# Performance work log

Measured on AMD Instinct MI355X. Metric: run time of the kernel, lower is better.

Reference implementation:

```python
import jax, jax.numpy as jnp
import numpy as np

NUM_HEADS = 16
EMBED_DIM = 1024
HEAD_DIM = EMBED_DIM // NUM_HEADS
REG_LEN = 2048
SUM_LEN = 64
BSZ = 2
REL_DIM = 64
NUM_REL_EMB = 64
MAX_SUMMARY = 64
SCALE = HEAD_DIM ** -0.5


def _ln(x, g, b, eps=1e-5):
    m = jnp.mean(x, axis=-1, keepdims=True)
    v = jnp.mean((x - m) ** 2, axis=-1, keepdims=True)
    return (x - m) * jax.lax.rsqrt(v + eps) * g + b


def setup_inputs() -> dict:
    key = jax.random.key(0)
    ks = jax.random.split(key, 16)
    inp = {}
    inp['reg_x'] = jax.random.normal(ks[0], (REG_LEN, BSZ, EMBED_DIM), jnp.float32)
    inp['sum_token_ids'] = jax.random.randint(ks[1], (BSZ, SUM_LEN), 0, MAX_SUMMARY + 1)
    inp['rel_idx'] = jax.random.randint(ks[2], (BSZ, SUM_LEN + REG_LEN, REG_LEN), 0, NUM_REL_EMB)
    inp['sum_len'] = SUM_LEN
    inp['reg_len'] = REG_LEN
    emb = jax.random.normal(ks[3], (MAX_SUMMARY + 1, EMBED_DIM), jnp.float32) * 0.02
    inp['emb_sum'] = emb.at[0].set(0.0)  # padding_idx = 0
    inp['rel_emb0'] = jax.random.normal(ks[4], (NUM_REL_EMB, REL_DIM), jnp.float32) * 0.02

    def lin(k, din, dout):
        return jax.random.normal(k, (din, dout), jnp.float32) * (1.0 / np.sqrt(din))

    inp['Wq'] = lin(ks[5], EMBED_DIM, EMBED_DIM); inp['bq'] = jnp.zeros((EMBED_DIM,), jnp.float32)
    inp['Wk'] = lin(ks[6], EMBED_DIM, EMBED_DIM); inp['bk'] = jnp.zeros((EMBED_DIM,), jnp.float32)
    inp['Wv'] = lin(ks[7], EMBED_DIM, EMBED_DIM); inp['bv'] = jnp.zeros((EMBED_DIM,), jnp.float32)
    inp['Wr0'] = lin(ks[8], REL_DIM, EMBED_DIM); inp['br0'] = jnp.zeros((EMBED_DIM,), jnp.float32)
    inp['Wk2'] = lin(ks[9], HEAD_DIM, HEAD_DIM); inp['bk2'] = jnp.zeros((HEAD_DIM,), jnp.float32)
    inp['Wv2'] = lin(ks[10], HEAD_DIM, HEAD_DIM); inp['bv2'] = jnp.zeros((HEAD_DIM,), jnp.float32)
    inp['Wo'] = lin(ks[11], EMBED_DIM, EMBED_DIM); inp['bo'] = jnp.zeros((EMBED_DIM,), jnp.float32)
    for name in ['ln_k', 'ln_v', 'ln_k2', 'ln_v2']:
        inp[name + '_g'] = jnp.ones((HEAD_DIM,), jnp.float32)
        inp[name + '_b'] = jnp.zeros((HEAD_DIM,), jnp.float32)
    return inp


def reference(reg_x, sum_token_ids, rel_idx, sum_len, reg_len, emb_sum, rel_emb0,
              Wq, bq, Wk, bk, Wv, bv, Wr0, br0, Wk2, bk2, Wv2, bv2, Wo, bo,
              ln_k_g, ln_k_b, ln_v_g, ln_v_b, ln_k2_g, ln_k2_b, ln_v2_g, ln_v2_b):
    R, B, E = reg_x.shape  # reg_len, bsz, embed_dim
    H, D = NUM_HEADS, HEAD_DIM
    S = sum_token_ids.shape[1]

    # regular K/V projections + per-head LayerNorm
    reg_k = _ln((reg_x @ Wk + bk).reshape(R, B, H, D), ln_k_g, ln_k_b)
    reg_v = _ln((reg_x @ Wv + bv).reshape(R, B, H, D), ln_v_g, ln_v_b)

    # relation-type embedding projection -> [Rrel, H, D]
    r0 = (rel_emb0 @ Wr0 + br0).reshape(NUM_REL_EMB, H, D)

    # --- stage 1: summary tokens attend over regular tokens ---
    sum_x = emb_sum[sum_token_ids.T]                     # [S, B, E]
    sum_q = sum_x.reshape(S, B, H, D) * SCALE
    scores_sum = jnp.einsum('sbhd,kbhd->bhsk', sum_q, reg_k)   # [B,H,S,R]
    qr_sum = jnp.einsum('sbhd,Zhd->bhsZ', sum_q, r0)           # [B,H,S,Rrel]
    idx_sum = rel_idx[:, :S]                                   # [B,S,R]
    scores_sum = scores_sum + jnp.take_along_axis(qr_sum, idx_sum[:, None, :, :], axis=-1)
    w_sum = jax.nn.softmax(scores_sum, axis=-1)
    sum_x2 = jnp.einsum('bhsk,kbhd->sbhd', w_sum, reg_v)       # [S,B,H,D]

    sum_k2 = _ln(sum_x2 @ Wk2 + bk2, ln_k2_g, ln_k2_b)
    sum_v2 = _ln(sum_x2 @ Wv2 + bv2, ln_v2_g, ln_v2_b)

    # --- stage 2: regular tokens attend over [summary ; regular] keys ---
    reg_q = (reg_x @ Wq + bq).reshape(R, B, H, D) * SCALE
    scores_rs = jnp.einsum('qbhd,sbhd->bhqs', reg_q, sum_k2)   # [B,H,R,S]
    scores_rr = jnp.einsum('qbhd,kbhd->bhqk', reg_q, reg_k)    # [B,H,R,R]
    qr_reg = jnp.einsum('qbhd,Zhd->bhqZ', reg_q, r0)
    idx_reg = rel_idx[:, S:]                                   # [B,R,R]
    scores_rr = scores_rr + jnp.take_along_axis(qr_reg, idx_reg[:, None, :, :], axis=-1)
    scores = jnp.concatenate([scores_rs, scores_rr], axis=-1)  # [B,H,R,S+R]
    w = jax.nn.softmax(scores, axis=-1)
    v_all = jnp.concatenate([sum_v2, reg_v], axis=0)           # [S+R,B,H,D]
    attn_out = jnp.einsum('bhqk,kbhd->qbhd', w, v_all).reshape(R, B, E)
    reg_x2 = attn_out @ Wo + bo
    return reg_x2
```

## Files before the change

kernel.cpp:

```cpp
#include <hip/hip_runtime.h>
#include <cstdint>
#include <cstddef>

#define NH   16
#define HD   64
#define RLEN 2048
#define BSZ  2
#define SLEN 64
#define NZ   64
#define ED   1024
#define KTOT 2112
#define NSPLIT 8

typedef __bf16 bf16_t;
typedef bf16_t bf16x8 __attribute__((ext_vector_type(8)));
typedef bf16_t bf16x4 __attribute__((ext_vector_type(4)));
typedef float  f32x4  __attribute__((ext_vector_type(4)));

__device__ __forceinline__ f32x4 mfma16(bf16x8 a, bf16x8 b, f32x4 c) {
    return __builtin_amdgcn_mfma_f32_16x16x32_bf16(a, b, c, 0, 0, 0);
}

__device__ __forceinline__ void dma16(const void* g, void* l) {
    __builtin_amdgcn_global_load_lds(
        (const __attribute__((address_space(1))) unsigned int*)g,
        (__attribute__((address_space(3))) unsigned int*)l, 16, 0, 0);
}


template<int BM>
__global__ __launch_bounds__(256) void gemm_fast(
    const bf16_t* __restrict__ A, const bf16_t* __restrict__ Bt,
    const float* __restrict__ b0, const float* __restrict__ b1,
    const float* __restrict__ b2,
    bf16_t* __restrict__ oq, float* __restrict__ o1, float* __restrict__ o2,
    int M, int K, int N, int mode)
{
    constexpr int MT = BM / 64;
    __shared__ __align__(16) bf16_t As[BM * 64];
    __shared__ __align__(16) bf16_t Bs[128 * 64];

    const int t = threadIdx.x;
    const int wave = t >> 6, lane = t & 63;
    const int quad = lane >> 4, l15 = lane & 15;
    const int rsub = lane >> 3, gq = lane & 7;
    const int m0 = blockIdx.y * BM, n0 = blockIdx.x * 128;

    f32x4 acc[MT][8];
#pragma unroll
    for (int i = 0; i < MT; i++)
#pragma unroll
        for (int j = 0; j < 8; j++) acc[i][j] = (f32x4){0.f, 0.f, 0.f, 0.f};

    for (int k0 = 0; k0 < K; k0 += 64) {
#pragma unroll
        for (int j = 0; j < BM / 32; j++) {
            int row = wave * (BM / 4) + j * 8 + rsub;
            const bf16_t* g = A + (size_t)(m0 + row) * K + k0 + ((gq ^ (row & 7)) * 8);
            dma16(g, As + (wave * (BM / 4) + j * 8) * 64);
        }
#pragma unroll
        for (int j = 0; j < 4; j++) {
            int row = wave * 32 + j * 8 + rsub;
            const bf16_t* g = Bt + (size_t)(n0 + row) * K + k0 + ((gq ^ (row & 7)) * 8);
            dma16(g, Bs + (wave * 32 + j * 8) * 64);
        }
        __syncthreads();

#pragma unroll
        for (int kk = 0; kk < 2; kk++) {
            const int pg = ((kk * 4 + quad) ^ (l15 & 7)) * 8;
            bf16x8 af[MT], bf[8];
#pragma unroll
            for (int mt = 0; mt < MT; mt++)
                af[mt] = *(const bf16x8*)(As + (wave * (BM / 4) + mt * 16 + l15) * 64 + pg);
#pragma unroll
            for (int nt = 0; nt < 8; nt++)
                bf[nt] = *(const bf16x8*)(Bs + (nt * 16 + l15) * 64 + pg);
#pragma unroll
            for (int mt = 0; mt < MT; mt++)
#pragma unroll
                for (int nt = 0; nt < 8; nt++)
                    acc[mt][nt] = mfma16(af[mt], bf[nt], acc[mt][nt]);
        }
        __syncthreads();
    }

#pragma unroll
    for (int mt = 0; mt < MT; mt++)
#pragma unroll
        for (int nt = 0; nt < 8; nt++)
#pragma unroll
            for (int reg = 0; reg < 4; reg++) {
                int m = m0 + wave * (BM / 4) + mt * 16 + quad * 4 + reg;
                int n = n0 + nt * 16 + l15;
                if (mode == 0) {
                    o1[(size_t)m * N + n] = acc[mt][nt][reg] + b0[n];
                } else {
                    int seg = n >> 10, nl = n & 1023;
                    const float* bias = (seg == 0) ? b0 : (seg == 1) ? b1 : b2;
                    float c = acc[mt][nt][reg] + bias[nl];
                    int h = nl >> 6, d = nl & 63;
                    int r = m >> 1, bb = m & 1;
                    size_t off = (((size_t)bb * NH + h) * RLEN + r) * HD + d;
                    if (seg == 0)      oq[off] = (bf16_t)(c * 0.125f);
                    else if (seg == 1) o1[off] = c;
                    else               o2[off] = c;
                }
            }
}

__global__ __launch_bounds__(256) void gemm_mfma(
    const bf16_t* __restrict__ A, const bf16_t* __restrict__ Bt,
    const float* __restrict__ bias, float* __restrict__ outf,
    int M, int K, int N, int Rr)
{
    constexpr int LDA = 40;
    __shared__ __align__(16) bf16_t As[64 * LDA];
    __shared__ __align__(16) bf16_t Bs[128 * LDA];

    const int t = threadIdx.x;
    const int wave = t >> 6, lane = t & 63;
    const int quad = lane >> 4, l15 = lane & 15;
    const int wrow = wave >> 1, wcol = wave & 1;
    const int m0 = blockIdx.y * 64, n0 = blockIdx.x * 128;

    f32x4 acc[2][4];
#pragma unroll
    for (int i = 0; i < 2; i++)
#pragma unroll
        for (int j = 0; j < 4; j++) acc[i][j] = (f32x4){0.f, 0.f, 0.f, 0.f};

    const int srow = t >> 2, sseg = (t & 3) * 8;

    for (int k0 = 0; k0 < K; k0 += 32) {
        bf16x8 av  = *(const bf16x8*)(A  + (size_t)(m0 + srow) * K + k0 + sseg);
        bf16x8 bv0 = *(const bf16x8*)(Bt + (size_t)(n0 + srow) * K + k0 + sseg);
        bf16x8 bv1 = *(const bf16x8*)(Bt + (size_t)(n0 + 64 + srow) * K + k0 + sseg);
        __syncthreads();
        *(bf16x8*)(As + srow * LDA + sseg)        = av;
        *(bf16x8*)(Bs + srow * LDA + sseg)        = bv0;
        *(bf16x8*)(Bs + (64 + srow) * LDA + sseg) = bv1;
        __syncthreads();

        bf16x8 af[2], bf[4];
#pragma unroll
        for (int mt = 0; mt < 2; mt++)
            af[mt] = *(const bf16x8*)(As + (wrow * 32 + mt * 16 + l15) * LDA + quad * 8);
#pragma unroll
        for (int nt = 0; nt < 4; nt++)
            bf[nt] = *(const bf16x8*)(Bs + (wcol * 64 + nt * 16 + l15) * LDA + quad * 8);
#pragma unroll
        for (int mt = 0; mt < 2; mt++)
#pragma unroll
            for (int nt = 0; nt < 4; nt++)
                acc[mt][nt] = mfma16(af[mt], bf[nt], acc[mt][nt]);
    }

#pragma unroll
    for (int mt = 0; mt < 2; mt++)
#pragma unroll
        for (int nt = 0; nt < 4; nt++)
#pragma unroll
            for (int reg = 0; reg < 4; reg++) {
                int m = m0 + wrow * 32 + mt * 16 + quad * 4 + reg;
                int n = n0 + wcol * 64 + nt * 16 + l15;
                if (m >= M) continue;
                float c = acc[mt][nt][reg] + bias[n];
                int h = n >> 6, d = n & 63;
                outf[(((size_t)h) * Rr + m) * HD + d] = c;
            }
}

__global__ __launch_bounds__(256) void ln_k_frag(
    const float* __restrict__ x, const float* __restrict__ g, const float* __restrict__ b,
    bf16_t* __restrict__ kfm)
{
    int row  = blockIdx.x * 4 + (threadIdx.x >> 6);
    int lane = threadIdx.x & 63;
    float v = x[(size_t)row * HD + lane];
    float s1 = v, s2 = v * v;
#pragma unroll
    for (int o = 32; o > 0; o >>= 1) {
        s1 += __shfl_xor(s1, o);
        s2 += __shfl_xor(s2, o);
    }
    float mean = s1 * (1.f / 64.f);
    float var  = s2 * (1.f / 64.f) - mean * mean;
    float y = (v - mean) * rsqrtf(var + 1e-5f) * g[lane] + b[lane];
    int bh = row >> 11, r = row & 2047, d = lane;
    int rt = r & 63;
    size_t off = (size_t)bh * 131072 + (size_t)(r >> 6) * 4096 +
        (size_t)((((rt & 3) * 2 + (d >> 5)) * 64 + ((d >> 3) & 3) * 16 + (rt >> 2)) * 8 + (d & 7));
    kfm[off] = (bf16_t)y;
}

__global__ __launch_bounds__(256) void lnv_frag(
    const float* __restrict__ v, const float* __restrict__ g,
    const float* __restrict__ b, bf16_t* __restrict__ vfm)
{
    __shared__ float tile[64][65];
    const int bh = blockIdx.y, tidx = blockIdx.x;
    const int t = threadIdx.x;
    const int wave = t >> 6, lane = t & 63;

#pragma unroll
    for (int i = 0; i < 16; i++) {
        int rl = wave * 16 + i;
        float x = v[((size_t)bh * RLEN + tidx * 64 + rl) * HD + lane];
        float s1 = x, s2 = x * x;
#pragma unroll
        for (int o = 32; o > 0; o >>= 1) {
            s1 += __shfl_xor(s1, o);
            s2 += __shfl_xor(s2, o);
        }
        float mean = s1 * (1.f / 64.f);
        float var  = s2 * (1.f / 64.f) - mean * mean;
        tile[rl][lane] = (x - mean) * rsqrtf(var + 1e-5f) * g[lane] + b[lane];
    }
    __syncthreads();
    int d = t >> 2, rs = (t & 3) * 16;
    bf16x8 o0, o1;
#pragma unroll
    for (int j = 0; j < 8; j++) {
        o0[j] = (bf16_t)tile[rs + j][d];
        o1[j] = (bf16_t)tile[rs + 8 + j][d];
    }
    size_t base = (size_t)bh * 131072;
    size_t off0 = base + (size_t)((((tidx * 4 + (d >> 4)) * 2 + (rs >> 5)) * 64
                  + ((rs >> 3) & 3) * 16 + (d & 15)) * 8);
    int rs2 = rs + 8;
    size_t off1 = base + (size_t)((((tidx * 4 + (d >> 4)) * 2 + (rs2 >> 5)) * 64
                  + ((rs2 >> 3) & 3) * 16 + (d & 15)) * 8);
    *(bf16x8*)(vfm + off0) = o0;
    *(bf16x8*)(vfm + off1) = o1;
}

__global__ __launch_bounds__(256) void cvt_bf16(
    const float* __restrict__ src, bf16_t* __restrict__ dst, int n)
{
    int i = (blockIdx.x * 256 + threadIdx.x) * 4;
    if (i < n) {
        float4 v = *(const float4*)(src + i);
        bf16x4 o;
        o[0] = (bf16_t)v.x; o[1] = (bf16_t)v.y; o[2] = (bf16_t)v.z; o[3] = (bf16_t)v.w;
        *(bf16x4*)(dst + i) = o;
    }
}

__global__ __launch_bounds__(256) void wt_batch(
    const float* __restrict__ Wq, const float* __restrict__ Wk,
    const float* __restrict__ Wv, const float* __restrict__ Wo,
    const float* __restrict__ Wr0,
    bf16_t* __restrict__ wqt, bf16_t* __restrict__ wkt,
    bf16_t* __restrict__ wvt, bf16_t* __restrict__ wot,
    bf16_t* __restrict__ wr0t)
{
    __shared__ float tile[64][65];
    const int bid = blockIdx.x;
    const float* src; bf16_t* dst; int R, C, r0, c0;
    if (bid < 1024) {
        int sel = bid >> 8, local = bid & 255;
        src = (sel == 0) ? Wq : (sel == 1) ? Wk : (sel == 2) ? Wv : Wo;
        dst = (sel == 0) ? wqt : (sel == 1) ? wkt : (sel == 2) ? wvt : wot;
        R = ED; C = ED; r0 = (local >> 4) * 64; c0 = (local & 15) * 64;
    } else {
        src = Wr0; dst = wr0t; R = NZ; C = ED; r0 = 0; c0 = (bid - 1024) * 64;
    }
    const int t = threadIdx.x;
#pragma unroll
    for (int i = 0; i < 4; i++) {
        int idx = t + i * 256;
        int r = idx >> 4, c = (idx & 15) * 4;
        float4 vv = *(const float4*)(src + (size_t)(r0 + r) * C + c0 + c);
        tile[r][c] = vv.x; tile[r][c + 1] = vv.y; tile[r][c + 2] = vv.z; tile[r][c + 3] = vv.w;
    }
    __syncthreads();
    int cc = t >> 2, rs = (t & 3) * 16;
    bf16x8 o0, o1;
#pragma unroll
    for (int j = 0; j < 8; j++) {
        o0[j] = (bf16_t)tile[rs + j][cc];
        o1[j] = (bf16_t)tile[rs + 8 + j][cc];
    }
    *(bf16x8*)(dst + (size_t)(c0 + cc) * R + r0 + rs) = o0;
    *(bf16x8*)(dst + (size_t)(c0 + cc) * R + r0 + rs + 8) = o1;
}

__global__ __launch_bounds__(256) void sumq_gather(
    const float* __restrict__ emb, const int* __restrict__ ids,
    bf16_t* __restrict__ sum_q)
{
    int sb = blockIdx.x;
    int s = sb >> 1, b = sb & 1;
    int id = ids[b * SLEN + s];
    const float* src = emb + (size_t)id * ED;
    for (int e = threadIdx.x; e < ED; e += 256) {
        int h = e >> 6, d = e & 63;
        sum_q[(((size_t)b * NH + h) * SLEN + s) * HD + d] = (bf16_t)(src[e] * 0.125f);
    }
}

__device__ __forceinline__ void attn_tile(
    const bf16_t* __restrict__ kt, const bf16_t* __restrict__ vt,
    const int* __restrict__ rp0, const int* __restrict__ rp1,
    const int* __restrict__ rp2, const int* __restrict__ rp3,
    bool userel,
    const float* __restrict__ qrsw, bf16_t* __restrict__ Psw,
    bf16x8 qf0, bf16x8 qf1,
    f32x4 (&O)[4], float (&m_i)[4], float (&l_i)[4],
    int quad, int l15, int lane)
{
    bf16x8 kf[4][2];
#pragma unroll
    for (int nt = 0; nt < 4; nt++)
#pragma unroll
        for (int kb = 0; kb < 2; kb++)
            kf[nt][kb] = *(const bf16x8*)(kt + ((nt * 2 + kb) * 64 + lane) * 8);

    int4 crel[4];
    if (userel) {
        crel[0] = *(const int4*)rp0;
        crel[1] = *(const int4*)rp1;
        crel[2] = *(const int4*)rp2;
        crel[3] = *(const int4*)rp3;
    }

    f32x4 S[4];
#pragma unroll
    for (int nt = 0; nt < 4; nt++) {
        f32x4 acc = (f32x4){0.f, 0.f, 0.f, 0.f};
        acc = mfma16(qf0, kf[nt][0], acc);
        acc = mfma16(qf1, kf[nt][1], acc);
        S[nt] = acc;
    }

    bf16x8 vf[4][2];
#pragma unroll
    for (int nt = 0; nt < 4; nt++)
#pragma unroll
        for (int kb = 0; kb < 2; kb++)
            vf[nt][kb] = *(const bf16x8*)(vt + ((nt * 2 + kb) * 64 + lane) * 8);

    if (userel) {
#pragma unroll
        for (int reg = 0; reg < 4; reg++) {
            const float* qr = qrsw + (quad * 4 + reg) * 64;
            int4 c = crel[reg];
            S[0][reg] += qr[c.x];
            S[1][reg] += qr[c.y];
            S[2][reg] += qr[c.z];
            S[3][reg] += qr[c.w];
        }
    }

    float tmax[4];
#pragma unroll
    for (int reg = 0; reg < 4; reg++) {
        float v = fmaxf(fmaxf(S[0][reg], S[1][reg]), fmaxf(S[2][reg], S[3][reg]));
#pragma unroll
        for (int o = 8; o > 0; o >>= 1) v = fmaxf(v, __shfl_xor(v, o));
        tmax[reg] = v;
    }
    float alpha[4], psum[4];
#pragma unroll
    for (int reg = 0; reg < 4; reg++) {
        float mn = fmaxf(m_i[reg], tmax[reg]);
        alpha[reg] = __expf(m_i[reg] - mn);
        m_i[reg] = mn;
        psum[reg] = 0.f;
    }
#pragma unroll
    for (int nt = 0; nt < 4; nt++)
#pragma unroll
        for (int reg = 0; reg < 4; reg++) {
            float p = __expf(S[nt][reg] - m_i[reg]);
            S[nt][reg] = p;
            psum[reg] += p;
        }
#pragma unroll
    for (int reg = 0; reg < 4; reg++) {
#pragma unroll
        for (int o = 8; o > 0; o >>= 1) psum[reg] += __shfl_xor(psum[reg], o);
        l_i[reg] = l_i[reg] * alpha[reg] + psum[reg];
    }
#pragma unroll
    for (int nt = 0; nt < 4; nt++) {
        O[nt][0] *= alpha[0]; O[nt][1] *= alpha[1];
        O[nt][2] *= alpha[2]; O[nt][3] *= alpha[3];
    }

#pragma unroll
    for (int reg = 0; reg < 4; reg++) {
        bf16x4 pv;
        pv[0] = (bf16_t)S[0][reg]; pv[1] = (bf16_t)S[1][reg];
        pv[2] = (bf16_t)S[2][reg]; pv[3] = (bf16_t)S[3][reg];
        *(bf16x4*)(Psw + (quad * 4 + reg) * 72 + 4 * l15) = pv;
    }
    bf16x8 pf0 = *(const bf16x8*)(Psw + l15 * 72 + quad * 8);
    bf16x8 pf1 = *(const bf16x8*)(Psw + l15 * 72 + 32 + quad * 8);
#pragma unroll
    for (int nt = 0; nt < 4; nt++) {
        O[nt] = mfma16(pf0, vf[nt][0], O[nt]);
        O[nt] = mfma16(pf1, vf[nt][1], O[nt]);
    }
}

__device__ __forceinline__ void build_qr(
    const float* __restrict__ r0, int h, bf16x8 qf0, bf16x8 qf1,
    float* __restrict__ qrsw, int quad, int l15)
{
#pragma unroll
    for (int nt = 0; nt < 4; nt++) {
        const float* rp = r0 + ((size_t)h * NZ + l15 + 16 * nt) * HD + quad * 8;
        float4 a0 = *(const float4*)(rp);
        float4 a1 = *(const float4*)(rp + 4);
        bf16x8 bf0;
        bf0[0] = (bf16_t)a0.x; bf0[1] = (bf16_t)a0.y; bf0[2] = (bf16_t)a0.z; bf0[3] = (bf16_t)a0.w;
        bf0[4] = (bf16_t)a1.x; bf0[5] = (bf16_t)a1.y; bf0[6] = (bf16_t)a1.z; bf0[7] = (bf16_t)a1.w;
        float4 b0 = *(const float4*)(rp + 32);
        float4 b1 = *(const float4*)(rp + 36);
        bf16x8 bf1;
        bf1[0] = (bf16_t)b0.x; bf1[1] = (bf16_t)b0.y; bf1[2] = (bf16_t)b0.z; bf1[3] = (bf16_t)b0.w;
        bf1[4] = (bf16_t)b1.x; bf1[5] = (bf16_t)b1.y; bf1[6] = (bf16_t)b1.z; bf1[7] = (bf16_t)b1.w;
        f32x4 qa = (f32x4){0.f, 0.f, 0.f, 0.f};
        qa = mfma16(qf0, bf0, qa);
        qa = mfma16(qf1, bf1, qa);
#pragma unroll
        for (int reg = 0; reg < 4; reg++)
            qrsw[(quad * 4 + reg) * 64 + l15 + 16 * nt] = qa[reg];
    }
}

__global__ __launch_bounds__(256) void sum_attn_split(
    const bf16_t* __restrict__ Qb,
    const bf16_t* __restrict__ kfm, const bf16_t* __restrict__ vfm,
    const float*  __restrict__ r0,
    const int*    __restrict__ rel_idx,
    float* __restrict__ po, float* __restrict__ pm, float* __restrict__ pl)
{
    const int bh = blockIdx.x;
    const int split = blockIdx.y;
    const int b = bh >> 4, h = bh & 15;
    const int t = threadIdx.x;
    const int wave = t >> 6, lane = t & 63;
    const int quad = lane >> 4, l15 = lane & 15;

    __shared__ __align__(16) bf16_t Ps[4][16 * 72];
    __shared__ float qrs[4][16 * 64];

    const bf16_t* Qrow = Qb + ((size_t)bh * SLEN + wave * 16 + l15) * HD;
    bf16x8 qf0 = *(const bf16x8*)(Qrow + quad * 8);
    bf16x8 qf1 = *(const bf16x8*)(Qrow + 32 + quad * 8);

    build_qr(r0, h, qf0, qf1, qrs[wave], quad, l15);

    f32x4 O[4];
    float m_i[4], l_i[4];
#pragma unroll
    for (int nt = 0; nt < 4; nt++) O[nt] = (f32x4){0.f, 0.f, 0.f, 0.f};
#pragma unroll
    for (int r = 0; r < 4; r++) { m_i[r] = -1e30f; l_i[r] = 0.f; }

    const int* relp[4];
#pragma unroll
    for (int reg = 0; reg < 4; reg++)
        relp[reg] = rel_idx + ((size_t)b * KTOT + wave * 16 + quad * 4 + reg) * RLEN + 4 * l15;

    const bf16_t* kbase = kfm + (size_t)bh * 131072 + (size_t)(split * 4) * 4096;
    const bf16_t* vbase = vfm + (size_t)bh * 131072 + (size_t)(split * 4) * 4096;

    for (int i = 0; i < 4; i++) {
        const int koff = (split * 4 + i) * 64;
        attn_tile(kbase + (size_t)i * 4096, vbase + (size_t)i * 4096,
                  relp[0] + koff, relp[1] + koff, relp[2] + koff, relp[3] + koff, true,
                  qrs[wave], Ps[wave], qf0, qf1, O, m_i, l_i, quad, l15, lane);
    }

    const size_t pslot = (size_t)bh * NSPLIT + split;
#pragma unroll
    for (int nt = 0; nt < 4; nt++)
#pragma unroll
        for (int reg = 0; reg < 4; reg++) {
            int sq = wave * 16 + quad * 4 + reg;
            po[(pslot * SLEN + sq) * HD + l15 + 16 * nt] = O[nt][reg];
        }
#pragma unroll
    for (int reg = 0; reg < 4; reg++) {
        int sq = wave * 16 + quad * 4 + reg;
        if (l15 == 0) {
            pm[pslot * SLEN + sq] = m_i[reg];
            pl[pslot * SLEN + sq] = l_i[reg];
        }
    }
}

__global__ __launch_bounds__(256) void sum_reduce(
    const float* __restrict__ po, const float* __restrict__ pm,
    const float* __restrict__ pl, float* __restrict__ sum_x2)
{
    const int bh = blockIdx.x;
    const int sg0 = blockIdx.y * 16;
    const int t = threadIdx.x;
    const int d = t & 63, si = t >> 6;
#pragma unroll
    for (int i = 0; i < 4; i++) {
        int s = sg0 + si * 4 + i;
        float M = -1e30f, mm[NSPLIT];
#pragma unroll
        for (int j = 0; j < NSPLIT; j++) {
            mm[j] = pm[((size_t)bh * NSPLIT + j) * SLEN + s];
            M = fmaxf(M, mm[j]);
        }
        float L = 0.f, acc = 0.f;
#pragma unroll
        for (int j = 0; j < NSPLIT; j++) {
            float a = __expf(mm[j] - M);
            L += pl[((size_t)bh * NSPLIT + j) * SLEN + s] * a;
            acc += po[(((size_t)bh * NSPLIT + j) * SLEN + s) * HD + d] * a;
        }
        sum_x2[((size_t)bh * SLEN + s) * HD + d] = acc / L;
    }
}

__global__ __launch_bounds__(64) void k2v2(
    const float* __restrict__ sum_x2,
    const float* __restrict__ Wk2, const float* __restrict__ bk2,
    const float* __restrict__ Wv2, const float* __restrict__ bv2,
    const float* __restrict__ gk, const float* __restrict__ bk,
    const float* __restrict__ gv, const float* __restrict__ bv,
    bf16_t* __restrict__ k2fm, bf16_t* __restrict__ v2fm)
{
    int row = blockIdx.x;
    int d = threadIdx.x;
    int bh = row >> 6, s = row & 63;
    __shared__ float xs[64];
    xs[d] = sum_x2[(size_t)row * HD + d];
    __syncthreads();

#pragma unroll
    for (int which = 0; which < 2; which++) {
        const float* W  = which ? Wv2 : Wk2;
        const float* bi = which ? bv2 : bk2;
        const float* g  = which ? gv : gk;
        const float* bb = which ? bv : bk;
        float a = bi[d];
#pragma unroll
        for (int j = 0; j < 64; j++) a += xs[j] * W[j * HD + d];
        float s1 = a, s2 = a * a;
#pragma unroll
        for (int o = 32; o > 0; o >>= 1) {
            s1 += __shfl_xor(s1, o);
            s2 += __shfl_xor(s2, o);
        }
        float mean = s1 * (1.f / 64.f);
        float var  = s2 * (1.f / 64.f) - mean * mean;
        float y = (a - mean) * rsqrtf(var + 1e-5f) * g[d] + bb[d];
        if (which == 0) {
            size_t off = (size_t)bh * 4096 +
                (size_t)((((s & 3) * 2 + (d >> 5)) * 64
                          + ((d >> 3) & 3) * 16 + (s >> 2)) * 8 + (d & 7));
            k2fm[off] = (bf16_t)y;
        } else {
            size_t off = (size_t)bh * 4096 +
                (size_t)((((d >> 4) * 2 + (s >> 5)) * 64
                          + ((s >> 3) & 3) * 16 + (d & 15)) * 8 + (s & 7));
            v2fm[off] = (bf16_t)y;
        }
    }
}

__global__ __launch_bounds__(256) void reg_attn_mfma(
    const bf16_t* __restrict__ Qb,
    const bf16_t* __restrict__ kfm, const bf16_t* __restrict__ vfm,
    const bf16_t* __restrict__ k2fm, const bf16_t* __restrict__ v2fm,
    const float*  __restrict__ r0,
    const int*    __restrict__ rel_idx,
    bf16_t* __restrict__ attn_out)
{
    const int bid = blockIdx.x;
    const int bh = (bid & 7) * 4 + ((bid >> 3) & 3);
    const int qt = bid >> 5;
    const int b = bh >> 4, h = bh & 15;
    const int q0 = qt * 64;

    const int t = threadIdx.x;
    const int wave = t >> 6, lane = t & 63;
    const int quad = lane >> 4, l15 = lane & 15;

    __shared__ __align__(16) bf16_t Ps[4][16 * 72];
    __shared__ float qrs[4][16 * 64];

    const bf16_t* Qrow = Qb + ((size_t)bh * RLEN + q0 + wave * 16 + l15) * HD;
    bf16x8 qf0 = *(const bf16x8*)(Qrow + quad * 8);
    bf16x8 qf1 = *(const bf16x8*)(Qrow + 32 + quad * 8);

    build_qr(r0, h, qf0, qf1, qrs[wave], quad, l15);

    f32x4 O[4];
    float m_i[4], l_i[4];
#pragma unroll
    for (int nt = 0; nt < 4; nt++) O[nt] = (f32x4){0.f, 0.f, 0.f, 0.f};
#pragma unroll
    for (int r = 0; r < 4; r++) { m_i[r] = -1e30f; l_i[r] = 0.f; }

    const int* relp[4];
#pragma unroll
    for (int reg = 0; reg < 4; reg++)
        relp[reg] = rel_idx +
            ((size_t)b * KTOT + SLEN + q0 + wave * 16 + quad * 4 + reg) * RLEN + 4 * l15;

    attn_tile(k2fm + (size_t)bh * 4096, v2fm + (size_t)bh * 4096,
              nullptr, nullptr, nullptr, nullptr, false,
              qrs[wave], Ps[wave], qf0, qf1, O, m_i, l_i, quad, l15, lane);

    const bf16_t* kt = kfm + (size_t)bh * 131072;
    const bf16_t* vt = vfm + (size_t)bh * 131072;
    for (int tile = 0; tile < 32; tile++) {
        const int koff = tile * 64;
        attn_tile(kt, vt,
                  relp[0] + koff, relp[1] + koff, relp[2] + koff, relp[3] + koff, true,
                  qrs[wave], Ps[wave], qf0, qf1, O, m_i, l_i, quad, l15, lane);
        kt += 4096; vt += 4096;
    }

    float linv[4];
#pragma unroll
    for (int reg = 0; reg < 4; reg++) linv[reg] = 1.0f / l_i[reg];
#pragma unroll
    for (int nt = 0; nt < 4; nt++)
#pragma unroll
        for (int reg = 0; reg < 4; reg++) {
            int q = q0 + wave * 16 + quad * 4 + reg;
            attn_out[((size_t)q * BSZ + b) * ED + h * HD + l15 + 16 * nt] =
                (bf16_t)(O[nt][reg] * linv[reg]);
        }
}

extern "C" void kernel_launch(void* const* d_in, const int* in_sizes, int n_in,
                              void* d_out, int out_size, void* d_ws, size_t ws_size,
                              hipStream_t stream)
{
    const float* reg_x    = (const float*)d_in[0];
    const int*   sum_ids  = (const int*)d_in[1];
    const int*   rel_idx  = (const int*)d_in[2];
    const float* emb_sum  = (const float*)d_in[5];
    const float* rel_emb0 = (const float*)d_in[6];
    const float* Wq = (const float*)d_in[7];
    const float* bq = (const float*)d_in[8];
    const float* Wk = (const float*)d_in[9];
    const float* bk = (const float*)d_in[10];
    const float* Wv = (const float*)d_in[11];
    const float* bv = (const float*)d_in[12];
    const float* Wr0 = (const float*)d_in[13];
    const float* br0 = (const float*)d_in[14];
    const float* Wk2 = (const float*)d_in[15];
    const float* bk2 = (const float*)d_in[16];
    const float* Wv2 = (const float*)d_in[17];
    const float* bv2 = (const float*)d_in[18];
    const float* Wo  = (const float*)d_in[19];
    const float* bo  = (const float*)d_in[20];
    const float* ln_k_g  = (const float*)d_in[21];
    const float* ln_k_b  = (const float*)d_in[22];
    const float* ln_v_g  = (const float*)d_in[23];
    const float* ln_v_b  = (const float*)d_in[24];
    const float* ln_k2_g = (const float*)d_in[25];
    const float* ln_k2_b = (const float*)d_in[26];
    const float* ln_v2_g = (const float*)d_in[27];
    const float* ln_v2_b = (const float*)d_in[28];

    const size_t QKV = (size_t)BSZ * NH * RLEN * HD;
    const size_t SUM = (size_t)BSZ * NH * SLEN * HD;

    float* ws  = (float*)d_ws;
    float* k   = ws;
    float* v   = k + QKV;
    float* r0  = v + QKV;
    float* sx2 = r0 + (size_t)NH * NZ * HD;

    bf16_t* xb   = (bf16_t*)(sx2 + SUM);
    bf16_t* qb   = xb + QKV;
    bf16_t* kfm  = qb + QKV;
    bf16_t* vfm  = kfm + QKV;
    bf16_t* sqb  = vfm + QKV;
    bf16_t* k2fm = sqb + SUM;
    bf16_t* v2fm = k2fm + SUM;
    bf16_t* wqt  = v2fm + SUM;
    bf16_t* wkt  = wqt + (size_t)ED * ED;
    bf16_t* wvt  = wkt + (size_t)ED * ED;
    bf16_t* wot  = wvt + (size_t)ED * ED;
    bf16_t* wr0t = wot + (size_t)ED * ED;
    bf16_t* re0b = wr0t + (size_t)ED * NZ;
    bf16_t* aob  = (bf16_t*)k;
    float*  po   = (float*)xb;
    float*  pm   = po + (size_t)BSZ * NH * NSPLIT * SLEN * HD;
    float*  pl   = pm + (size_t)BSZ * NH * NSPLIT * SLEN;

    const int M = RLEN * BSZ;

    cvt_bf16<<<(int)(QKV / 1024), 256, 0, stream>>>(reg_x, xb, (int)QKV);
    cvt_bf16<<<4, 256, 0, stream>>>(rel_emb0, re0b, NZ * NZ);
    wt_batch<<<1040, 256, 0, stream>>>(Wq, Wk, Wv, Wo, Wr0, wqt, wkt, wvt, wot, wr0t);

    gemm_fast<128><<<dim3(3 * ED / 128, M / 128), 256, 0, stream>>>(
        xb, wqt, bq, bk, bv, qb, k, v, M, ED, 3 * ED, 1);

    ln_k_frag<<<(BSZ * NH * RLEN) / 4, 256, 0, stream>>>(k, ln_k_g, ln_k_b, kfm);
    lnv_frag<<<dim3(RLEN / 64, BSZ * NH), 256, 0, stream>>>(v, ln_v_g, ln_v_b, vfm);

    gemm_mfma<<<dim3(ED / 128, 1), 256, 0, stream>>>(re0b, wr0t, br0, r0, NZ, NZ, ED, NZ);

    sumq_gather<<<SLEN * BSZ, 256, 0, stream>>>(emb_sum, sum_ids, sqb);

    sum_attn_split<<<dim3(BSZ * NH, NSPLIT), 256, 0, stream>>>(sqb, kfm, vfm, r0, rel_idx, po, pm, pl);
    sum_reduce<<<dim3(BSZ * NH, 4), 256, 0, stream>>>(po, pm, pl, sx2);

    k2v2<<<BSZ * NH * SLEN, 64, 0, stream>>>(sx2, Wk2, bk2, Wv2, bv2,
                                             ln_k2_g, ln_k2_b, ln_v2_g, ln_v2_b, k2fm, v2fm);

    reg_attn_mfma<<<1024, 256, 0, stream>>>(qb, kfm, vfm, k2fm, v2fm, r0, rel_idx, aob);

    gemm_fast<64><<<dim3(ED / 128, M / 64), 256, 0, stream>>>(
        aob, wot, bo, nullptr, nullptr, nullptr, (float*)d_out, nullptr, M, ED, ED, 0);
}
```

Measured before the change: 417.6 us.

## Process two query tiles per wave, share row max, fuse small prep kernels

The regular attention kernel now handles 32 query rows per wave (two 16-row MFMA tiles), so each K/V fragment load is reused across twice the queries and the grid is halved. Online softmax uses a single running max per wave instead of per row, and row sums are computed with an MFMA against a ones vector instead of shuffle reductions. The sum_q gather and rel_emb conversion are merged into the weight-transpose launch, and sum_reduce is fused into k2v2, removing several launches. Register pressure rises and occupancy falls. The shared max across 32 rows risks underflow when row maxima differ widely.

Measured after the change: 366.4 us. 12.2% less time.

```diff
diff --git a/kernel.cpp b/kernel.cpp
--- a/kernel.cpp
+++ b/kernel.cpp
@@ -248,16 +248,41 @@
     }
 }
 
-__global__ __launch_bounds__(256) void wt_batch(
+__global__ __launch_bounds__(256) void prep_batch(
     const float* __restrict__ Wq, const float* __restrict__ Wk,
     const float* __restrict__ Wv, const float* __restrict__ Wo,
     const float* __restrict__ Wr0,
     bf16_t* __restrict__ wqt, bf16_t* __restrict__ wkt,
     bf16_t* __restrict__ wvt, bf16_t* __restrict__ wot,
-    bf16_t* __restrict__ wr0t)
-{
+    bf16_t* __restrict__ wr0t,
+    const float* __restrict__ emb, const int* __restrict__ ids,
+    bf16_t* __restrict__ sum_q,
+    const float* __restrict__ rel_emb0, bf16_t* __restrict__ re0b)
+{
+    const int bid = blockIdx.x;
+    const int t = threadIdx.x;
+
+    if (bid >= 1168) {
+        int i = ((bid - 1168) * 256 + t) * 4;
+        float4 v = *(const float4*)(rel_emb0 + i);
+        bf16x4 o;
+        o[0] = (bf16_t)v.x; o[1] = (bf16_t)v.y; o[2] = (bf16_t)v.z; o[3] = (bf16_t)v.w;
+        *(bf16x4*)(re0b + i) = o;
+        return;
+    }
+    if (bid >= 1040) {
+        int sb = bid - 1040;
+        int s = sb >> 1, b = sb & 1;
+        int id = ids[b * SLEN + s];
+        const float* src = emb + (size_t)id * ED;
+        for (int e = t; e < ED; e += 256) {
+            int h = e >> 6, d = e & 63;
+            sum_q[(((size_t)b * NH + h) * SLEN + s) * HD + d] = (bf16_t)(src[e] * 0.125f);
+        }
+        return;
+    }
+
     __shared__ float tile[64][65];
-    const int bid = blockIdx.x;
     const float* src; bf16_t* dst; int R, C, r0, c0;
     if (bid < 1024) {
         int sel = bid >> 8, local = bid & 255;
@@ -267,7 +292,6 @@
     } else {
         src = Wr0; dst = wr0t; R = NZ; C = ED; r0 = 0; c0 = (bid - 1024) * 64;
     }
-    const int t = threadIdx.x;
 #pragma unroll
     for (int i = 0; i < 4; i++) {
         int idx = t + i * 256;
@@ -287,28 +311,13 @@
     *(bf16x8*)(dst + (size_t)(c0 + cc) * R + r0 + rs + 8) = o1;
 }
 
-__global__ __launch_bounds__(256) void sumq_gather(
-    const float* __restrict__ emb, const int* __restrict__ ids,
-    bf16_t* __restrict__ sum_q)
-{
-    int sb = blockIdx.x;
-    int s = sb >> 1, b = sb & 1;
-    int id = ids[b * SLEN + s];
-    const float* src = emb + (size_t)id * ED;
-    for (int e = threadIdx.x; e < ED; e += 256) {
-        int h = e >> 6, d = e & 63;
-        sum_q[(((size_t)b * NH + h) * SLEN + s) * HD + d] = (bf16_t)(src[e] * 0.125f);
-    }
-}
-
+template<int MT>
 __device__ __forceinline__ void attn_tile(
     const bf16_t* __restrict__ kt, const bf16_t* __restrict__ vt,
-    const int* __restrict__ rp0, const int* __restrict__ rp1,
-    const int* __restrict__ rp2, const int* __restrict__ rp3,
-    bool userel,
+    const int* __restrict__ relbase, int koff, bool userel,
     const float* __restrict__ qrsw, bf16_t* __restrict__ Psw,
-    bf16x8 qf0, bf16x8 qf1,
-    f32x4 (&O)[4], float (&m_i)[4], float (&l_i)[4],
+    const bf16x8 (&qf)[MT][2],
+    f32x4 (&O)[MT][4], float& m_q, float (&l_i)[MT][4],
     int quad, int l15, int lane)
 {
     bf16x8 kf[4][2];
@@ -318,22 +327,25 @@
         for (int kb = 0; kb < 2; kb++)
             kf[nt][kb] = *(const bf16x8*)(kt + ((nt * 2 + kb) * 64 + lane) * 8);
 
-    int4 crel[4];
+    int4 crel[MT][4];
     if (userel) {
-        crel[0] = *(const int4*)rp0;
-        crel[1] = *(const int4*)rp1;
-        crel[2] = *(const int4*)rp2;
-        crel[3] = *(const int4*)rp3;
-    }
-
-    f32x4 S[4];
-#pragma unroll
-    for (int nt = 0; nt < 4; nt++) {
-        f32x4 acc = (f32x4){0.f, 0.f, 0.f, 0.f};
-        acc = mfma16(qf0, kf[nt][0], acc);
-        acc = mfma16(qf1, kf[nt][1], acc);
-        S[nt] = acc;
-    }
+#pragma unroll
+        for (int mt = 0; mt < MT; mt++)
+#pragma unroll
+            for (int reg = 0; reg < 4; reg++)
+                crel[mt][reg] = *(const int4*)(relbase + (size_t)(mt * 16 + reg) * RLEN + koff);
+    }
+
+    f32x4 S[MT][4];
+#pragma unroll
+    for (int mt = 0; mt < MT; mt++)
+#pragma unroll
+        for (int nt = 0; nt < 4; nt++) {
+            f32x4 acc = (f32x4){0.f, 0.f, 0.f, 0.f};
+            acc = mfma16(qf[mt][0], kf[nt][0], acc);
+            acc = mfma16(qf[mt][1], kf[nt][1], acc);
+            S[mt][nt] = acc;
+        }
 
     bf16x8 vf[4][2];
 #pragma unroll
@@ -344,70 +356,85 @@
 
     if (userel) {
 #pragma unroll
+        for (int mt = 0; mt < MT; mt++)
+#pragma unroll
+            for (int reg = 0; reg < 4; reg++) {
+                const float* qr = qrsw + (mt * 16 + quad * 4 + reg) * 64;
+                int4 c = crel[mt][reg];
+                S[mt][0][reg] += qr[c.x];
+                S[mt][1][reg] += qr[c.y];
+                S[mt][2][reg] += qr[c.z];
+                S[mt][3][reg] += qr[c.w];
+            }
+    }
+
+    float v = -1e30f;
+#pragma unroll
+    for (int mt = 0; mt < MT; mt++)
+#pragma unroll
+        for (int nt = 0; nt < 4; nt++) {
+            f32x4 s = S[mt][nt];
+            v = fmaxf(v, fmaxf(fmaxf(s[0], s[1]), fmaxf(s[2], s[3])));
+        }
+#pragma unroll
+    for (int o = 8; o > 0; o >>= 1) v = fmaxf(v, __shfl_xor(v, o));
+    float mnew = fmaxf(m_q, v);
+    float alpha = __expf(m_q - mnew);
+    m_q = mnew;
+
+#pragma unroll
+    for (int mt = 0; mt < MT; mt++)
+#pragma unroll
+        for (int nt = 0; nt < 4; nt++)
+#pragma unroll
+            for (int reg = 0; reg < 4; reg++)
+                S[mt][nt][reg] = __expf(S[mt][nt][reg] - mnew);
+
+#pragma unroll
+    for (int mt = 0; mt < MT; mt++) {
+#pragma unroll
+        for (int nt = 0; nt < 4; nt++) {
+            O[mt][nt][0] *= alpha; O[mt][nt][1] *= alpha;
+            O[mt][nt][2] *= alpha; O[mt][nt][3] *= alpha;
+        }
+#pragma unroll
+        for (int reg = 0; reg < 4; reg++) l_i[mt][reg] *= alpha;
+    }
+
+    bf16x8 ones;
+#pragma unroll
+    for (int j = 0; j < 8; j++) ones[j] = (bf16_t)1.0f;
+
+#pragma unroll
+    for (int mt = 0; mt < MT; mt++)
+#pragma unroll
         for (int reg = 0; reg < 4; reg++) {
-            const float* qr = qrsw + (quad * 4 + reg) * 64;
-            int4 c = crel[reg];
-            S[0][reg] += qr[c.x];
-            S[1][reg] += qr[c.y];
-            S[2][reg] += qr[c.z];
-            S[3][reg] += qr[c.w];
-        }
-    }
-
-    float tmax[4];
-#pragma unroll
-    for (int reg = 0; reg < 4; reg++) {
-        float v = fmaxf(fmaxf(S[0][reg], S[1][reg]), fmaxf(S[2][reg], S[3][reg]));
-#pragma unroll
-        for (int o = 8; o > 0; o >>= 1) v = fmaxf(v, __shfl_xor(v, o));
-        tmax[reg] = v;
-    }
-    float alpha[4], psum[4];
-#pragma unroll
-    for (int reg = 0; reg < 4; reg++) {
-        float mn = fmaxf(m_i[reg], tmax[reg]);
-        alpha[reg] = __expf(m_i[reg] - mn);
-        m_i[reg] = mn;
-        psum[reg] = 0.f;
-    }
-#pragma unroll
-    for (int nt = 0; nt < 4; nt++)
-#pragma unroll
-        for (int reg = 0; reg < 4; reg++) {
-            float p = __expf(S[nt][reg] - m_i[reg]);
-            S[nt][reg] = p;
-            psum[reg] += p;
-        }
-#pragma unroll
-    for (int reg = 0; reg < 4; reg++) {
-#pragma unroll
-        for (int o = 8; o > 0; o >>= 1) psum[reg] += __shfl_xor(psum[reg], o);
-        l_i[reg] = l_i[reg] * alpha[reg] + psum[reg];
-    }
-#pragma unroll
-    for (int nt = 0; nt < 4; nt++) {
-        O[nt][0] *= alpha[0]; O[nt][1] *= alpha[1];
-        O[nt][2] *= alpha[2]; O[nt][3] *= alpha[3];
-    }
-
-#pragma unroll
-    for (int reg = 0; reg < 4; reg++) {
-        bf16x4 pv;
-        pv[0] = (bf16_t)S[0][reg]; pv[1] = (bf16_t)S[1][reg];
-        pv[2] = (bf16_t)S[2][reg]; pv[3] = (bf16_t)S[3][reg];
-        *(bf16x4*)(Psw + (quad * 4 + reg) * 72 + 4 * l15) = pv;
-    }
-    bf16x8 pf0 = *(const bf16x8*)(Psw + l15 * 72 + quad * 8);
-    bf16x8 pf1 = *(const bf16x8*)(Psw + l15 * 72 + 32 + quad * 8);
-#pragma unroll
-    for (int nt = 0; nt < 4; nt++) {
-        O[nt] = mfma16(pf0, vf[nt][0], O[nt]);
-        O[nt] = mfma16(pf1, vf[nt][1], O[nt]);
-    }
-}
-
+            bf16x4 pv;
+            pv[0] = (bf16_t)S[mt][0][reg]; pv[1] = (bf16_t)S[mt][1][reg];
+            pv[2] = (bf16_t)S[mt][2][reg]; pv[3] = (bf16_t)S[mt][3][reg];
+            *(bf16x4*)(Psw + (mt * 16 + quad * 4 + reg) * 72 + 4 * l15) = pv;
+        }
+
+#pragma unroll
+    for (int mt = 0; mt < MT; mt++) {
+        bf16x8 pf0 = *(const bf16x8*)(Psw + (mt * 16 + l15) * 72 + quad * 8);
+        bf16x8 pf1 = *(const bf16x8*)(Psw + (mt * 16 + l15) * 72 + 32 + quad * 8);
+        f32x4 ls = (f32x4){0.f, 0.f, 0.f, 0.f};
+        ls = mfma16(pf0, ones, ls);
+        ls = mfma16(pf1, ones, ls);
+#pragma unroll
+        for (int nt = 0; nt < 4; nt++) {
+            O[mt][nt] = mfma16(pf0, vf[nt][0], O[mt][nt]);
+            O[mt][nt] = mfma16(pf1, vf[nt][1], O[mt][nt]);
+        }
+#pragma unroll
+        for (int reg = 0; reg < 4; reg++) l_i[mt][reg] += ls[reg];
+    }
+}
+
+template<int MT>
 __device__ __forceinline__ void build_qr(
-    const float* __restrict__ r0, int h, bf16x8 qf0, bf16x8 qf1,
+    const float* __restrict__ r0, int h, const bf16x8 (&qf)[MT][2],
     float* __restrict__ qrsw, int quad, int l15)
 {
 #pragma unroll
@@ -423,12 +450,15 @@
         bf16x8 bf1;
         bf1[0] = (bf16_t)b0.x; bf1[1] = (bf16_t)b0.y; bf1[2] = (bf16_t)b0.z; bf1[3] = (bf16_t)b0.w;
         bf1[4] = (bf16_t)b1.x; bf1[5] = (bf16_t)b1.y; bf1[6] = (bf16_t)b1.z; bf1[7] = (bf16_t)b1.w;
-        f32x4 qa = (f32x4){0.f, 0.f, 0.f, 0.f};
-        qa = mfma16(qf0, bf0, qa);
-        qa = mfma16(qf1, bf1, qa);
-#pragma unroll
-        for (int reg = 0; reg < 4; reg++)
-            qrsw[(quad * 4 + reg) * 64 + l15 + 16 * nt] = qa[reg];
+#pragma unroll
+        for (int mt = 0; mt < MT; mt++) {
+            f32x4 qa = (f32x4){0.f, 0.f, 0.f, 0.f};
+            qa = mfma16(qf[mt][0], bf0, qa);
+            qa = mfma16(qf[mt][1], bf1, qa);
+#pragma unroll
+            for (int reg = 0; reg < 4; reg++)
+                qrsw[(mt * 16 + quad * 4 + reg) * 64 + l15 + 16 * nt] = qa[reg];
+        }
     }
 }
 
@@ -449,32 +479,31 @@
     __shared__ __align__(16) bf16_t Ps[4][16 * 72];
     __shared__ float qrs[4][16 * 64];
 
+    bf16x8 qf[1][2];
     const bf16_t* Qrow = Qb + ((size_t)bh * SLEN + wave * 16 + l15) * HD;
-    bf16x8 qf0 = *(const bf16x8*)(Qrow + quad * 8);
-    bf16x8 qf1 = *(const bf16x8*)(Qrow + 32 + quad * 8);
-
-    build_qr(r0, h, qf0, qf1, qrs[wave], quad, l15);
-
-    f32x4 O[4];
-    float m_i[4], l_i[4];
-#pragma unroll
-    for (int nt = 0; nt < 4; nt++) O[nt] = (f32x4){0.f, 0.f, 0.f, 0.f};
-#pragma unroll
-    for (int r = 0; r < 4; r++) { m_i[r] = -1e30f; l_i[r] = 0.f; }
-
-    const int* relp[4];
-#pragma unroll
-    for (int reg = 0; reg < 4; reg++)
-        relp[reg] = rel_idx + ((size_t)b * KTOT + wave * 16 + quad * 4 + reg) * RLEN + 4 * l15;
+    qf[0][0] = *(const bf16x8*)(Qrow + quad * 8);
+    qf[0][1] = *(const bf16x8*)(Qrow + 32 + quad * 8);
+
+    build_qr<1>(r0, h, qf, qrs[wave], quad, l15);
+
+    f32x4 O[1][4];
+    float m_q = -1e30f;
+    float l_i[1][4];
+#pragma unroll
+    for (int nt = 0; nt < 4; nt++) O[0][nt] = (f32x4){0.f, 0.f, 0.f, 0.f};
+#pragma unroll
+    for (int r = 0; r < 4; r++) l_i[0][r] = 0.f;
+
+    const int* relbase = rel_idx + ((size_t)b * KTOT + wave * 16 + quad * 4) * RLEN + 4 * l15;
 
     const bf16_t* kbase = kfm + (size_t)bh * 131072 + (size_t)(split * 4) * 4096;
     const bf16_t* vbase = vfm + (size_t)bh * 131072 + (size_t)(split * 4) * 4096;
 
     for (int i = 0; i < 4; i++) {
         const int koff = (split * 4 + i) * 64;
-        attn_tile(kbase + (size_t)i * 4096, vbase + (size_t)i * 4096,
-                  relp[0] + koff, relp[1] + koff, relp[2] + koff, relp[3] + koff, true,
-                  qrs[wave], Ps[wave], qf0, qf1, O, m_i, l_i, quad, l15, lane);
+        attn_tile<1>(kbase + (size_t)i * 4096, vbase + (size_t)i * 4096,
+                     relbase, koff, true, qrs[wave], Ps[wave], qf,
+                     O, m_q, l_i, quad, l15, lane);
     }
 
     const size_t pslot = (size_t)bh * NSPLIT + split;
@@ -483,48 +512,21 @@
 #pragma unroll
         for (int reg = 0; reg < 4; reg++) {
             int sq = wave * 16 + quad * 4 + reg;
-            po[(pslot * SLEN + sq) * HD + l15 + 16 * nt] = O[nt][reg];
+            po[(pslot * SLEN + sq) * HD + l15 + 16 * nt] = O[0][nt][reg];
         }
 #pragma unroll
     for (int reg = 0; reg < 4; reg++) {
         int sq = wave * 16 + quad * 4 + reg;
         if (l15 == 0) {
-            pm[pslot * SLEN + sq] = m_i[reg];
-            pl[pslot * SLEN + sq] = l_i[reg];
-        }
-    }
-}
-
-__global__ __launch_bounds__(256) void sum_reduce(
+            pm[pslot * SLEN + sq] = m_q;
+            pl[pslot * SLEN + sq] = l_i[0][reg];
+        }
+    }
+}
+
+__global__ __launch_bounds__(64) void k2v2_fused(
     const float* __restrict__ po, const float* __restrict__ pm,
-    const float* __restrict__ pl, float* __restrict__ sum_x2)
-{
-    const int bh = blockIdx.x;
-    const int sg0 = blockIdx.y * 16;
-    const int t = threadIdx.x;
-    const int d = t & 63, si = t >> 6;
-#pragma unroll
-    for (int i = 0; i < 4; i++) {
-        int s = sg0 + si * 4 + i;
-        float M = -1e30f, mm[NSPLIT];
-#pragma unroll
-        for (int j = 0; j < NSPLIT; j++) {
-            mm[j] = pm[((size_t)bh * NSPLIT + j) * SLEN + s];
-            M = fmaxf(M, mm[j]);
-        }
-        float L = 0.f, acc = 0.f;
-#pragma unroll
-        for (int j = 0; j < NSPLIT; j++) {
-            float a = __expf(mm[j] - M);
-            L += pl[((size_t)bh * NSPLIT + j) * SLEN + s] * a;
-            acc += po[(((size_t)bh * NSPLIT + j) * SLEN + s) * HD + d] * a;
-        }
-        sum_x2[((size_t)bh * SLEN + s) * HD + d] = acc / L;
-    }
-}
-
-__global__ __launch_bounds__(64) void k2v2(
-    const float* __restrict__ sum_x2,
+    const float* __restrict__ pl,
     const float* __restrict__ Wk2, const float* __restrict__ bk2,
     const float* __restrict__ Wv2, const float* __restrict__ bv2,
     const float* __restrict__ gk, const float* __restrict__ bk,
@@ -534,8 +536,22 @@
     int row = blockIdx.x;
     int d = threadIdx.x;
     int bh = row >> 6, s = row & 63;
+
+    float M = -1e30f, mm[NSPLIT];
+#pragma unroll
+    for (int j = 0; j < NSPLIT; j++) {
+        mm[j] = pm[((size_t)bh * NSPLIT + j) * SLEN + s];
+        M = fmaxf(M, mm[j]);
+    }
+    float L = 0.f, acc = 0.f;
+#pragma unroll
+    for (int j = 0; j < NSPLIT; j++) {
+        float a = __expf(mm[j] - M);
+        L += pl[((size_t)bh * NSPLIT + j) * SLEN + s] * a;
+        acc += po[(((size_t)bh * NSPLIT + j) * SLEN + s) * HD + d] * a;
+    }
     __shared__ float xs[64];
-    xs[d] = sum_x2[(size_t)row * HD + d];
+    xs[d] = acc / L;
     __syncthreads();
 
 #pragma unroll
@@ -582,59 +598,66 @@
     const int bh = (bid & 7) * 4 + ((bid >> 3) & 3);
     const int qt = bid >> 5;
     const int b = bh >> 4, h = bh & 15;
-    const int q0 = qt * 64;
+    const int q0 = qt * 128;
 
     const int t = threadIdx.x;
     const int wave = t >> 6, lane = t & 63;
     const int quad = lane >> 4, l15 = lane & 15;
 
-    __shared__ __align__(16) bf16_t Ps[4][16 * 72];
-    __shared__ float qrs[4][16 * 64];
-
-    const bf16_t* Qrow = Qb + ((size_t)bh * RLEN + q0 + wave * 16 + l15) * HD;
-    bf16x8 qf0 = *(const bf16x8*)(Qrow + quad * 8);
-    bf16x8 qf1 = *(const bf16x8*)(Qrow + 32 + quad * 8);
-
-    build_qr(r0, h, qf0, qf1, qrs[wave], quad, l15);
-
-    f32x4 O[4];
-    float m_i[4], l_i[4];
-#pragma unroll
-    for (int nt = 0; nt < 4; nt++) O[nt] = (f32x4){0.f, 0.f, 0.f, 0.f};
-#pragma unroll
-    for (int r = 0; r < 4; r++) { m_i[r] = -1e30f; l_i[r] = 0.f; }
-
-    const int* relp[4];
-#pragma unroll
-    for (int reg = 0; reg < 4; reg++)
-        relp[reg] = rel_idx +
-            ((size_t)b * KTOT + SLEN + q0 + wave * 16 + quad * 4 + reg) * RLEN + 4 * l15;
-
-    attn_tile(k2fm + (size_t)bh * 4096, v2fm + (size_t)bh * 4096,
-              nullptr, nullptr, nullptr, nullptr, false,
-              qrs[wave], Ps[wave], qf0, qf1, O, m_i, l_i, quad, l15, lane);
+    __shared__ __align__(16) bf16_t Ps[4][32 * 72];
+    __shared__ float qrs[4][32 * 64];
+
+    bf16x8 qf[2][2];
+#pragma unroll
+    for (int mt = 0; mt < 2; mt++) {
+        const bf16_t* Qrow = Qb + ((size_t)bh * RLEN + q0 + wave * 32 + mt * 16 + l15) * HD;
+        qf[mt][0] = *(const bf16x8*)(Qrow + quad * 8);
+        qf[mt][1] = *(const bf16x8*)(Qrow + 32 + quad * 8);
+    }
+
+    build_qr<2>(r0, h, qf, qrs[wave], quad, l15);
+
+    f32x4 O[2][4];
+    float m_q = -1e30f;
+    float l_i[2][4];
+#pragma unroll
+    for (int mt = 0; mt < 2; mt++)
+#pragma unroll
+        for (int nt = 0; nt < 4; nt++) O[mt][nt] = (f32x4){0.f, 0.f, 0.f, 0.f};
+#pragma unroll
+    for (int mt = 0; mt < 2; mt++)
+#pragma unroll
+        for (int r = 0; r < 4; r++) l_i[mt][r] = 0.f;
+
+    const int* relbase = rel_idx +
+        ((size_t)b * KTOT + SLEN + q0 + wave * 32 + quad * 4) * RLEN + 4 * l15;
+
+    attn_tile<2>(k2fm + (size_t)bh * 4096, v2fm + (size_t)bh * 4096,
+                 relbase, 0, false, qrs[wave], Ps[wave], qf,
+                 O, m_q, l_i, quad, l15, lane);
 
     const bf16_t* kt = kfm + (size_t)bh * 131072;
     const bf16_t* vt = vfm + (size_t)bh * 131072;
     for (int tile = 0; tile < 32; tile++) {
-        const int koff = tile * 64;
-        attn_tile(kt, vt,
-                  relp[0] + koff, relp[1] + koff, relp[2] + koff, relp[3] + koff, true,
-                  qrs[wave], Ps[wave], qf0, qf1, O, m_i, l_i, quad, l15, lane);
+        attn_tile<2>(kt, vt, relbase, tile * 64, true,
+                     qrs[wave], Ps[wave], qf, O, m_q, l_i, quad, l15, lane);
         kt += 4096; vt += 4096;
     }
 
-    float linv[4];
-#pragma unroll
-    for (int reg = 0; reg < 4; reg++) linv[reg] = 1.0f / l_i[reg];
-#pragma unroll
-    for (int nt = 0; nt < 4; nt++)
-#pragma unroll
-        for (int reg = 0; reg < 4; reg++) {
-            int q = q0 + wave * 16 + quad * 4 + reg;
-            attn_out[((size_t)q * BSZ + b) * ED + h * HD + l15 + 16 * nt] =
-                (bf16_t)(O[nt][reg] * linv[reg]);
-        }
+#pragma unroll
+    for (int mt = 0; mt < 2; mt++) {
+        float linv[4];
+#pragma unroll
+        for (int reg = 0; reg < 4; reg++) linv[reg] = 1.0f / l_i[mt][reg];
+#pragma unroll
+        for (int nt = 0; nt < 4; nt++)
+#pragma unroll
+            for (int reg = 0; reg < 4; reg++) {
+                int q = q0 + wave * 32 + mt * 16 + quad * 4 + reg;
+                attn_out[((size_t)q * BSZ + b) * ED + h * HD + l15 + 16 * nt] =
+                    (bf16_t)(O[mt][nt][reg] * linv[reg]);
+            }
+    }
 }
 
 extern "C" void kernel_launch(void* const* d_in, const int* in_sizes, int n_in,
@@ -676,9 +699,8 @@
     float* k   = ws;
     float* v   = k + QKV;
     float* r0  = v + QKV;
-    float* sx2 = r0 + (size_t)NH * NZ * HD;
-
-    bf16_t* xb   = (bf16_t*)(sx2 + SUM);
+
+    bf16_t* xb   = (bf16_t*)(r0 + (size_t)NH * NZ * HD);
     bf16_t* qb   = xb + QKV;
     bf16_t* kfm  = qb + QKV;
     bf16_t* vfm  = kfm + QKV;
@@ -699,8 +721,9 @@
     const int M = RLEN * BSZ;
 
     cvt_bf16<<<(int)(QKV / 1024), 256, 0, stream>>>(reg_x, xb, (int)QKV);
-    cvt_bf16<<<4, 256, 0, stream>>>(rel_emb0, re0b, NZ * NZ);
-    wt_batch<<<1040, 256, 0, stream>>>(Wq, Wk, Wv, Wo, Wr0, wqt, wkt, wvt, wot, wr0t);
+    prep_batch<<<1172, 256, 0, stream>>>(Wq, Wk, Wv, Wo, Wr0,
+                                         wqt, wkt, wvt, wot, wr0t,
+                                         emb_sum, sum_ids, sqb, rel_emb0, re0b);
 
     gemm_fast<128><<<dim3(3 * ED / 128, M / 128), 256, 0, stream>>>(
         xb, wqt, bq, bk, bv, qb, k, v, M, ED, 3 * ED, 1);
@@ -710,15 +733,13 @@
 
     gemm_mfma<<<dim3(ED / 128, 1), 256, 0, stream>>>(re0b, wr0t, br0, r0, NZ, NZ, ED, NZ);
 
-    sumq_gather<<<SLEN * BSZ, 256, 0, stream>>>(emb_sum, sum_ids, sqb);
-
     sum_attn_split<<<dim3(BSZ * NH, NSPLIT), 256, 0, stream>>>(sqb, kfm, vfm, r0, rel_idx, po, pm, pl);
-    sum_reduce<<<dim3(BSZ * NH, 4), 256, 0, stream>>>(po, pm, pl, sx2);
-
-    k2v2<<<BSZ * NH * SLEN, 64, 0, stream>>>(sx2, Wk2, bk2, Wv2, bv2,
-                                             ln_k2_g, ln_k2_b, ln_v2_g, ln_v2_b, k2fm, v2fm);
-
-    reg_attn_mfma<<<1024, 256, 0, stream>>>(qb, kfm, vfm, k2fm, v2fm, r0, rel_idx, aob);
+
+    k2v2_fused<<<BSZ * NH * SLEN, 64, 0, stream>>>(po, pm, pl, Wk2, bk2, Wv2, bv2,
+                                                   ln_k2_g, ln_k2_b, ln_v2_g, ln_v2_b,
+                                                   k2fm, v2fm);
+
+    reg_attn_mfma<<<512, 256, 0, stream>>>(qb, kfm, vfm, k2fm, v2fm, r0, rel_idx, aob);
 
     gemm_fast<64><<<dim3(ED / 128, M / 64), 256, 0, stream>>>(
         aob, wot, bo, nullptr, nullptr, nullptr, (float*)d_out, nullptr, M, ED, ED, 0);
```
